# Kernel optimization log

Measured on AMD Instinct MI355X. Metric: run time of the kernel, lower is better.

## Reference

```python
import jax, jax.numpy as jnp
import numpy as np

N_NODES = 50000
N_EDGES = 400000
IN_SIZE = 64
HID = 128


def _graph_conv(x, src, dst, W, b, n_nodes):
    """dgl-style GraphConv: gather src features, mean-aggregate at dst, then Linear."""
    msgs = x[src]                                            # [E, F] irregular gather
    agg = jax.ops.segment_sum(msgs, dst, num_segments=n_nodes)  # [N, F]
    deg = jax.ops.segment_sum(jnp.ones_like(dst, dtype=x.dtype), dst,
                              num_segments=n_nodes)
    agg = agg / jnp.maximum(deg, 1.0)[:, None]               # mean over in-neighbors
    return agg @ W + b


def setup_inputs() -> dict:
    key = jax.random.key(0)
    k1, k2, k3, k4, k5 = jax.random.split(key, 5)
    inputs = jax.random.normal(k1, (N_NODES, IN_SIZE), dtype=jnp.float32)
    states = jax.random.normal(k2, (N_NODES, HID), dtype=jnp.float32)
    edge_index = jax.random.randint(k3, (2, N_EDGES), 0, N_NODES, dtype=jnp.int32)
    fin = IN_SIZE + HID
    s1 = 1.0 / np.sqrt(fin)
    W_ru = jax.random.uniform(k4, (fin, 2 * HID), minval=-s1, maxval=s1, dtype=jnp.float32)
    b_ru = jnp.zeros((2 * HID,), dtype=jnp.float32)
    W_c = jax.random.uniform(k5, (fin, HID), minval=-s1, maxval=s1, dtype=jnp.float32)
    b_c = jnp.zeros((HID,), dtype=jnp.float32)
    return {"inputs": inputs, "states": states, "edge_index": edge_index,
            "W_ru": W_ru, "b_ru": b_ru, "W_c": W_c, "b_c": b_c}


def reference(inputs, states, edge_index, W_ru, b_ru, W_c, b_c):
    n = inputs.shape[0]
    src, dst = edge_index[0], edge_index[1]
    # r,u gates
    ru_in = jnp.concatenate([inputs, states], axis=-1)        # [N, in+hid]
    r_u = jax.nn.sigmoid(_graph_conv(ru_in, src, dst, W_ru, b_ru, n))  # [N, 2*hid]
    r, u = jnp.split(r_u, 2, axis=-1)
    # candidate
    c_in = jnp.concatenate([inputs, r * states], axis=-1)
    c = jnp.tanh(_graph_conv(c_in, src, dst, W_c, b_c, n))    # [N, hid]
    new_state = u * states + (1.0 - u) * c
    return (new_state, new_state)
```

## Files before the change

kernel.cpp:

```cpp
#include <hip/hip_runtime.h>
#include <hip/hip_bf16.h>
#include <math.h>

#define N_NODES 50000
#define N_EDGES 400000
#define F_IN    64
#define HID     128
#define FIN     192
#define RU      256
#define BCAP    128

#define COUNTS_OFF 0u
#define BKT_OFF    200064u
#define WRU_OFF    13000064u
#define WC_OFF     13098368u
#define SBF_OFF    13147520u
#define AX_OFF     25947520u
#define AS_OFF     32347520u
#define ARS_OFF    45147520u
#define RS2_OFF    57947520u
#define WS_NEED    70747520u

typedef __attribute__((ext_vector_type(8))) short short8;
typedef __attribute__((ext_vector_type(4))) float f32x4;

__device__ __forceinline__ float sigf(float x) { return 1.f / (1.f + expf(-x)); }
__device__ __forceinline__ float bf2f(unsigned short h) {
    return __uint_as_float(((unsigned)h) << 16);
}
__device__ __forceinline__ float bflo(unsigned v) { return __uint_as_float(v << 16); }
__device__ __forceinline__ float bfhi(unsigned v) { return __uint_as_float(v & 0xffff0000u); }
__device__ __forceinline__ unsigned short f2bf(float f) {
    unsigned u = __float_as_uint(f);
    return (unsigned short)((u + 0x7fff + ((u >> 16) & 1)) >> 16);
}
__device__ __forceinline__ unsigned packbf(float lo, float hi) {
    return ((unsigned)f2bf(hi) << 16) | (unsigned)f2bf(lo);
}

__global__ void k_fillb(const int* __restrict__ src, const int* __restrict__ dst,
                        int* __restrict__ counts, unsigned short* __restrict__ bkt) {
    const int e = blockIdx.x * 256 + threadIdx.x;
    if (e < N_EDGES) {
        const int d = dst[e];
        const int pos = atomicAdd(&counts[d], 1);
        if (pos < BCAP) bkt[(size_t)d * BCAP + pos] = (unsigned short)src[e];
    }
}

__global__ __launch_bounds__(256) void k_pre(
        const float* __restrict__ Wru, const float* __restrict__ Wc,
        unsigned short* __restrict__ Wru_bf, unsigned short* __restrict__ Wc_bf,
        const float* __restrict__ states, const float* __restrict__ inputs,
        uint2* __restrict__ s_bf2, uint2* __restrict__ x_bf2) {
    const int blk = blockIdx.x;
    if (blk < 288) {
        const int t = blk * 256 + threadIdx.x;
        if (t < FIN * RU) {
            const int k = t >> 8, c = t & 255;
            Wru_bf[c * FIN + k] = f2bf(Wru[t]);
        } else {
            const int tt = t - FIN * RU;
            const int k = tt >> 7, c = tt & 127;
            Wc_bf[c * FIN + k] = f2bf(Wc[tt]);
        }
    } else {
        const int t = (blk - 288) * 256 + threadIdx.x;
        if (t < N_NODES * HID / 4) {
            const float4 v = ((const float4*)states)[t];
            s_bf2[t] = make_uint2(packbf(v.x, v.y), packbf(v.z, v.w));
        } else {
            const int j = t - N_NODES * HID / 4;
            const float4 v = ((const float4*)inputs)[j];
            x_bf2[j] = make_uint2(packbf(v.x, v.y), packbf(v.z, v.w));
        }
    }
}

__global__ __launch_bounds__(256) void k_agg1(
        const unsigned short* __restrict__ bkt, const int* __restrict__ counts,
        const unsigned* __restrict__ x_u, const uint2* __restrict__ s_u2,
        unsigned* __restrict__ Ax_u, uint2* __restrict__ As_u2) {
    const int n = blockIdx.x * 4 + (threadIdx.x >> 6);
    const int lane = threadIdx.x & 63;
    const int half = lane >> 5;
    const int l = lane & 31;
    const int deg   = counts[n];
    const int start = n * BCAP;
    const int end   = start + (deg < BCAP ? deg : BCAP);
    float ax0 = 0.f, ax1 = 0.f, s0 = 0.f, s1 = 0.f, s2 = 0.f, s3 = 0.f;
    int e = start;
    for (; e + 8 <= end; e += 8) {
        const int ia = bkt[e + half];
        const int ib = bkt[e + 2 + half];
        const int ic = bkt[e + 4 + half];
        const int id = bkt[e + 6 + half];
        const unsigned xa = x_u[(size_t)ia * 32 + l];
        const uint2    sa = s_u2[(size_t)ia * 32 + l];
        const unsigned xb = x_u[(size_t)ib * 32 + l];
        const uint2    sb = s_u2[(size_t)ib * 32 + l];
        const unsigned xc = x_u[(size_t)ic * 32 + l];
        const uint2    sc = s_u2[(size_t)ic * 32 + l];
        const unsigned xd = x_u[(size_t)id * 32 + l];
        const uint2    sd = s_u2[(size_t)id * 32 + l];
        ax0 += bflo(xa); ax1 += bfhi(xa);
        s0 += bflo(sa.x); s1 += bfhi(sa.x); s2 += bflo(sa.y); s3 += bfhi(sa.y);
        ax0 += bflo(xb); ax1 += bfhi(xb);
        s0 += bflo(sb.x); s1 += bfhi(sb.x); s2 += bflo(sb.y); s3 += bfhi(sb.y);
        ax0 += bflo(xc); ax1 += bfhi(xc);
        s0 += bflo(sc.x); s1 += bfhi(sc.x); s2 += bflo(sc.y); s3 += bfhi(sc.y);
        ax0 += bflo(xd); ax1 += bfhi(xd);
        s0 += bflo(sd.x); s1 += bfhi(sd.x); s2 += bflo(sd.y); s3 += bfhi(sd.y);
    }
    if (e + 4 <= end) {
        const int ia = bkt[e + half];
        const int ib = bkt[e + 2 + half];
        const unsigned xa = x_u[(size_t)ia * 32 + l];
        const uint2    sa = s_u2[(size_t)ia * 32 + l];
        const unsigned xb = x_u[(size_t)ib * 32 + l];
        const uint2    sb = s_u2[(size_t)ib * 32 + l];
        ax0 += bflo(xa); ax1 += bfhi(xa);
        s0 += bflo(sa.x); s1 += bfhi(sa.x); s2 += bflo(sa.y); s3 += bfhi(sa.y);
        ax0 += bflo(xb); ax1 += bfhi(xb);
        s0 += bflo(sb.x); s1 += bfhi(sb.x); s2 += bflo(sb.y); s3 += bfhi(sb.y);
        e += 4;
    }
    if (e + 2 <= end) {
        const int ia = bkt[e + half];
        const unsigned xa = x_u[(size_t)ia * 32 + l];
        const uint2    sa = s_u2[(size_t)ia * 32 + l];
        ax0 += bflo(xa); ax1 += bfhi(xa);
        s0 += bflo(sa.x); s1 += bfhi(sa.x); s2 += bflo(sa.y); s3 += bfhi(sa.y);
        e += 2;
    }
    if (e < end && half == 0) {
        const int ia = bkt[e];
        const unsigned xa = x_u[(size_t)ia * 32 + l];
        const uint2    sa = s_u2[(size_t)ia * 32 + l];
        ax0 += bflo(xa); ax1 += bfhi(xa);
        s0 += bflo(sa.x); s1 += bfhi(sa.x); s2 += bflo(sa.y); s3 += bfhi(sa.y);
    }
    ax0 += __shfl_xor(ax0, 32); ax1 += __shfl_xor(ax1, 32);
    s0  += __shfl_xor(s0, 32);  s1  += __shfl_xor(s1, 32);
    s2  += __shfl_xor(s2, 32);  s3  += __shfl_xor(s3, 32);
    if (half == 0) {
        const float inv = 1.f / fmaxf((float)deg, 1.f);
        Ax_u[(size_t)n * 32 + l]  = packbf(ax0 * inv, ax1 * inv);
        As_u2[(size_t)n * 32 + l] = make_uint2(packbf(s0 * inv, s1 * inv),
                                               packbf(s2 * inv, s3 * inv));
    }
}

__global__ __launch_bounds__(256) void k_agg2(
        const unsigned short* __restrict__ bkt, const int* __restrict__ counts,
        const uint2* __restrict__ rs_u2, uint2* __restrict__ Ars_u2) {
    const int n = blockIdx.x * 4 + (threadIdx.x >> 6);
    const int lane = threadIdx.x & 63;
    const int half = lane >> 5;
    const int l = lane & 31;
    const int deg   = counts[n];
    const int start = n * BCAP;
    const int end   = start + (deg < BCAP ? deg : BCAP);
    float a0 = 0.f, a1 = 0.f, a2 = 0.f, a3 = 0.f;
    int e = start;
    for (; e + 8 <= end; e += 8) {
        const int ia = bkt[e + half];
        const int ib = bkt[e + 2 + half];
        const int ic = bkt[e + 4 + half];
        const int id = bkt[e + 6 + half];
        const uint2 va = rs_u2[(size_t)ia * 32 + l];
        const uint2 vb = rs_u2[(size_t)ib * 32 + l];
        const uint2 vc = rs_u2[(size_t)ic * 32 + l];
        const uint2 vd = rs_u2[(size_t)id * 32 + l];
        a0 += bflo(va.x); a1 += bfhi(va.x); a2 += bflo(va.y); a3 += bfhi(va.y);
        a0 += bflo(vb.x); a1 += bfhi(vb.x); a2 += bflo(vb.y); a3 += bfhi(vb.y);
        a0 += bflo(vc.x); a1 += bfhi(vc.x); a2 += bflo(vc.y); a3 += bfhi(vc.y);
        a0 += bflo(vd.x); a1 += bfhi(vd.x); a2 += bflo(vd.y); a3 += bfhi(vd.y);
    }
    if (e + 4 <= end) {
        const int ia = bkt[e + half];
        const int ib = bkt[e + 2 + half];
        const uint2 va = rs_u2[(size_t)ia * 32 + l];
        const uint2 vb = rs_u2[(size_t)ib * 32 + l];
        a0 += bflo(va.x); a1 += bfhi(va.x); a2 += bflo(va.y); a3 += bfhi(va.y);
        a0 += bflo(vb.x); a1 += bfhi(vb.x); a2 += bflo(vb.y); a3 += bfhi(vb.y);
        e += 4;
    }
    if (e + 2 <= end) {
        const int ia = bkt[e + half];
        const uint2 va = rs_u2[(size_t)ia * 32 + l];
        a0 += bflo(va.x); a1 += bfhi(va.x); a2 += bflo(va.y); a3 += bfhi(va.y);
        e += 2;
    }
    if (e < end && half == 0) {
        const int ia = bkt[e];
        const uint2 va = rs_u2[(size_t)ia * 32 + l];
        a0 += bflo(va.x); a1 += bfhi(va.x); a2 += bflo(va.y); a3 += bfhi(va.y);
    }
    a0 += __shfl_xor(a0, 32); a1 += __shfl_xor(a1, 32);
    a2 += __shfl_xor(a2, 32); a3 += __shfl_xor(a3, 32);
    if (half == 0) {
        const float inv = 1.f / fmaxf((float)deg, 1.f);
        Ars_u2[(size_t)n * 32 + l] = make_uint2(packbf(a0 * inv, a1 * inv),
                                                packbf(a2 * inv, a3 * inv));
    }
}

__global__ __launch_bounds__(256, 4) void k_gemm_r(
        const unsigned short* __restrict__ Ax, const unsigned short* __restrict__ As,
        const unsigned short* __restrict__ Wbf, const float* __restrict__ b,
        const unsigned short* __restrict__ s_bf, unsigned short* __restrict__ rs2) {
    __shared__ unsigned short Wt[64][200];
    const int t  = threadIdx.x;
    const int n0 = blockIdx.x * 128;
    const int colbase = blockIdx.y * 64;

    #pragma unroll
    for (int it = 0; it < 6; ++it) {
        const int task = t + 256 * it;
        const int c = task / 24, g = task - c * 24;
        *(uint4*)(&Wt[c][g * 8]) =
            *(const uint4*)(Wbf + (size_t)(colbase + c) * FIN + g * 8);
    }

    const int lane = t & 63, wave = t >> 6;
    const int fr = lane & 15;
    const int fk = (lane >> 4) * 8;

    short8 afr[2][6];
    const short8 zero = {};
    #pragma unroll
    for (int s = 0; s < 2; ++s) {
        const int n = n0 + wave * 32 + s * 16 + fr;
        if (n < N_NODES) {
            const unsigned short* axp = Ax + (size_t)n * F_IN + fk;
            const unsigned short* asp = As + (size_t)n * HID + fk;
            afr[s][0] = *(const short8*)(axp);
            afr[s][1] = *(const short8*)(axp + 32);
            afr[s][2] = *(const short8*)(asp);
            afr[s][3] = *(const short8*)(asp + 32);
            afr[s][4] = *(const short8*)(asp + 64);
            afr[s][5] = *(const short8*)(asp + 96);
        } else {
            #pragma unroll
            for (int j = 0; j < 6; ++j) afr[s][j] = zero;
        }
    }
    __syncthreads();

    f32x4 acc[2][4] = {};
    #pragma unroll
    for (int k0 = 0; k0 < 6; ++k0) {
        #pragma unroll
        for (int ct = 0; ct < 4; ++ct) {
            const short8 bw = *(const short8*)(&Wt[ct * 16 + fr][fk + k0 * 32]);
            acc[0][ct] = __builtin_amdgcn_mfma_f32_16x16x32_bf16(afr[0][k0], bw, acc[0][ct], 0, 0, 0);
            acc[1][ct] = __builtin_amdgcn_mfma_f32_16x16x32_bf16(afr[1][k0], bw, acc[1][ct], 0, 0, 0);
        }
    }

    #pragma unroll
    for (int s = 0; s < 2; ++s) {
        const int rbase = n0 + wave * 32 + s * 16 + (lane >> 4) * 4;
        #pragma unroll
        for (int ct = 0; ct < 4; ++ct) {
            const int col = colbase + ct * 16 + fr;
            const float bias = b[col];
            #pragma unroll
            for (int i = 0; i < 4; ++i) {
                const int n = rbase + i;
                if (n < N_NODES) {
                    const size_t idx = (size_t)n * HID + col;
                    const float r = sigf(acc[s][ct][i] + bias);
                    rs2[idx] = f2bf(r * bf2f(s_bf[idx]));
                }
            }
        }
    }
}

__global__ __launch_bounds__(256) void k_gemm_uc(
        const unsigned short* __restrict__ Ax, const unsigned short* __restrict__ As,
        const unsigned short* __restrict__ Ars,
        const unsigned short* __restrict__ Wru_bf, const unsigned short* __restrict__ Wc_bf,
        const float* __restrict__ b_ru, const float* __restrict__ b_c,
        const unsigned short* __restrict__ st_bf,
        float* __restrict__ out1, float* __restrict__ out2) {
    __shared__ unsigned short Wt[64][200];
    const int t  = threadIdx.x;
    const int n0 = blockIdx.x * 64;
    const int colbase = blockIdx.y * 64;
    const int lane = t & 63, wave = t >> 6;
    const int fr = lane & 15;
    const int fk = (lane >> 4) * 8;
    const int n = n0 + wave * 16 + fr;
    const short8 zero = {};

    #pragma unroll
    for (int it = 0; it < 6; ++it) {
        const int task = t + 256 * it;
        const int c = task / 24, g = task - c * 24;
        *(uint4*)(&Wt[c][g * 8]) =
            *(const uint4*)(Wru_bf + (size_t)(128 + colbase + c) * FIN + g * 8);
    }

    short8 axf0 = zero, axf1 = zero, sf[4] = {zero, zero, zero, zero};
    if (n < N_NODES) {
        const unsigned short* axp = Ax + (size_t)n * F_IN + fk;
        const unsigned short* asp = As + (size_t)n * HID + fk;
        axf0 = *(const short8*)(axp);
        axf1 = *(const short8*)(axp + 32);
        sf[0] = *(const short8*)(asp);
        sf[1] = *(const short8*)(asp + 32);
        sf[2] = *(const short8*)(asp + 64);
        sf[3] = *(const short8*)(asp + 96);
    }
    __syncthreads();

    f32x4 uacc[4] = {};
    #pragma unroll
    for (int k0 = 0; k0 < 6; ++k0) {
        const short8 a = (k0 == 0) ? axf0 : (k0 == 1) ? axf1 : sf[k0 - 2];
        #pragma unroll
        for (int ct = 0; ct < 4; ++ct) {
            const short8 bw = *(const short8*)(&Wt[ct * 16 + fr][fk + k0 * 32]);
            uacc[ct] = __builtin_amdgcn_mfma_f32_16x16x32_bf16(a, bw, uacc[ct], 0, 0, 0);
        }
    }
    float uu[4][4];
    #pragma unroll
    for (int ct = 0; ct < 4; ++ct) {
        const float bias = b_ru[128 + colbase + ct * 16 + fr];
        #pragma unroll
        for (int i = 0; i < 4; ++i) uu[ct][i] = sigf(uacc[ct][i] + bias);
    }
    __syncthreads();

    #pragma unroll
    for (int it = 0; it < 6; ++it) {
        const int task = t + 256 * it;
        const int c = task / 24, g = task - c * 24;
        *(uint4*)(&Wt[c][g * 8]) =
            *(const uint4*)(Wc_bf + (size_t)(colbase + c) * FIN + g * 8);
    }
    if (n < N_NODES) {
        const unsigned short* arp = Ars + (size_t)n * HID + fk;
        sf[0] = *(const short8*)(arp);
        sf[1] = *(const short8*)(arp + 32);
        sf[2] = *(const short8*)(arp + 64);
        sf[3] = *(const short8*)(arp + 96);
    }
    __syncthreads();

    f32x4 cacc[4] = {};
    #pragma unroll
    for (int k0 = 0; k0 < 6; ++k0) {
        const short8 a = (k0 == 0) ? axf0 : (k0 == 1) ? axf1 : sf[k0 - 2];
        #pragma unroll
        for (int ct = 0; ct < 4; ++ct) {
            const short8 bw = *(const short8*)(&Wt[ct * 16 + fr][fk + k0 * 32]);
            cacc[ct] = __builtin_amdgcn_mfma_f32_16x16x32_bf16(a, bw, cacc[ct], 0, 0, 0);
        }
    }

    const int rbase = n0 + wave * 16 + (lane >> 4) * 4;
    #pragma unroll
    for (int ct = 0; ct < 4; ++ct) {
        const int col = colbase + ct * 16 + fr;
        const float bias = b_c[col];
        #pragma unroll
        for (int i = 0; i < 4; ++i) {
            const int nn = rbase + i;
            if (nn < N_NODES) {
                const size_t idx = (size_t)nn * HID + col;
                const float c  = tanhf(cacc[ct][i] + bias);
                const float u  = uu[ct][i];
                const float st = bf2f(st_bf[idx]);
                const float ns = u * st + (1.f - u) * c;
                out1[idx] = ns;
                out2[idx] = ns;
            }
        }
    }
}

extern "C" void kernel_launch(void* const* d_in, const int* in_sizes, int n_in,
                              void* d_out, int out_size, void* d_ws, size_t ws_size,
                              hipStream_t stream) {
    const float* inputs = (const float*)d_in[0];
    const float* states = (const float*)d_in[1];
    const int*   ei     = (const int*)d_in[2];
    const float* W_ru   = (const float*)d_in[3];
    const float* b_ru   = (const float*)d_in[4];
    const float* W_c    = (const float*)d_in[5];
    const float* b_c    = (const float*)d_in[6];

    float* out  = (float*)d_out;
    float* out1 = out;
    float* out2 = out + (size_t)N_NODES * HID;

    char* ws = (char*)d_ws;
    int*            counts = (int*)(ws + COUNTS_OFF);
    unsigned short* bkt    = (unsigned short*)(ws + BKT_OFF);
    unsigned short* Wru_bf = (unsigned short*)(ws + WRU_OFF);
    unsigned short* Wc_bf  = (unsigned short*)(ws + WC_OFF);
    unsigned short* s_bf   = (unsigned short*)(ws + SBF_OFF);
    unsigned short* Ax     = (unsigned short*)(ws + AX_OFF);
    unsigned short* As     = (unsigned short*)(ws + AS_OFF);
    unsigned short* Ars    = (unsigned short*)(ws + ARS_OFF);
    unsigned short* rs2    = (unsigned short*)(ws + RS2_OFF);
    unsigned short* x_bf   = (unsigned short*)d_out;

    (void)ws_size;

    const int* src = ei;
    const int* dst = ei + N_EDGES;

    const int egrid      = (N_EDGES + 255) / 256;
    const int agg_grid   = N_NODES / 4;
    const int gr_grid    = (N_NODES + 127) / 128;
    const int guc_grid   = (N_NODES + 63) / 64;
    const int pre_grid   = 288 + (N_NODES * HID / 4 + N_NODES * F_IN / 4) / 256;

    hipMemsetAsync(counts, 0, N_NODES * sizeof(int), stream);
    k_fillb <<<egrid, 256, 0, stream>>>(src, dst, counts, bkt);
    k_pre   <<<pre_grid, 256, 0, stream>>>(W_ru, W_c, Wru_bf, Wc_bf, states, inputs,
                                           (uint2*)s_bf, (uint2*)x_bf);
    k_agg1  <<<agg_grid, 256, 0, stream>>>(bkt, counts, (const unsigned*)x_bf,
                                           (const uint2*)s_bf,
                                           (unsigned*)Ax, (uint2*)As);
    k_gemm_r<<<dim3(gr_grid, 2), 256, 0, stream>>>(Ax, As, Wru_bf, b_ru, s_bf, rs2);
    k_agg2  <<<agg_grid, 256, 0, stream>>>(bkt, counts, (const uint2*)rs2,
                                           (uint2*)Ars);
    k_gemm_uc<<<dim3(guc_grid, 2), 256, 0, stream>>>(Ax, As, Ars, Wru_bf, Wc_bf,
                                                     b_ru, b_c, s_bf, out1, out2);
}
```

Before: 141.2 us.

## Fuse bucket fill with preconversion kernel; double rows per block in gate GEMM

Merges the edge-bucketing kernel and the weight/feature bf16 conversion kernel into one launch, partitioned by block index, to save a launch and let the two run concurrently. Also makes k_gemm_uc process 128 nodes per block (two 16-row subtiles per wave), reusing each LDS weight tile across twice as many rows and halving the number of weight staging loads. The wider tile raises register use, which the added occupancy hint of 3 blocks per CU is meant to keep in check, and it reuses the u accumulators to hold the sigmoid values.

```diff
diff --git a/kernel.cpp b/kernel.cpp
--- a/kernel.cpp
+++ b/kernel.cpp
@@ -21,6 +21,10 @@
 #define RS2_OFF    57947520u
 #define WS_NEED    70747520u
 
+#define FILLB_BLKS 1563
+#define PREW_BLKS  288
+#define PREP_BLKS  9375
+
 typedef __attribute__((ext_vector_type(8))) short short8;
 typedef __attribute__((ext_vector_type(4))) float f32x4;
 
@@ -38,24 +42,23 @@
     return ((unsigned)f2bf(hi) << 16) | (unsigned)f2bf(lo);
 }
 
-__global__ void k_fillb(const int* __restrict__ src, const int* __restrict__ dst,
-                        int* __restrict__ counts, unsigned short* __restrict__ bkt) {
-    const int e = blockIdx.x * 256 + threadIdx.x;
-    if (e < N_EDGES) {
-        const int d = dst[e];
-        const int pos = atomicAdd(&counts[d], 1);
-        if (pos < BCAP) bkt[(size_t)d * BCAP + pos] = (unsigned short)src[e];
-    }
-}
-
-__global__ __launch_bounds__(256) void k_pre(
+__global__ __launch_bounds__(256) void k_fp(
+        const int* __restrict__ src, const int* __restrict__ dst,
+        int* __restrict__ counts, unsigned short* __restrict__ bkt,
         const float* __restrict__ Wru, const float* __restrict__ Wc,
         unsigned short* __restrict__ Wru_bf, unsigned short* __restrict__ Wc_bf,
         const float* __restrict__ states, const float* __restrict__ inputs,
         uint2* __restrict__ s_bf2, uint2* __restrict__ x_bf2) {
     const int blk = blockIdx.x;
-    if (blk < 288) {
-        const int t = blk * 256 + threadIdx.x;
+    if (blk < FILLB_BLKS) {
+        const int e = blk * 256 + threadIdx.x;
+        if (e < N_EDGES) {
+            const int d = dst[e];
+            const int pos = atomicAdd(&counts[d], 1);
+            if (pos < BCAP) bkt[(size_t)d * BCAP + pos] = (unsigned short)src[e];
+        }
+    } else if (blk < FILLB_BLKS + PREW_BLKS) {
+        const int t = (blk - FILLB_BLKS) * 256 + threadIdx.x;
         if (t < FIN * RU) {
             const int k = t >> 8, c = t & 255;
             Wru_bf[c * FIN + k] = f2bf(Wru[t]);
@@ -65,7 +68,7 @@
             Wc_bf[c * FIN + k] = f2bf(Wc[tt]);
         }
     } else {
-        const int t = (blk - 288) * 256 + threadIdx.x;
+        const int t = (blk - FILLB_BLKS - PREW_BLKS) * 256 + threadIdx.x;
         if (t < N_NODES * HID / 4) {
             const float4 v = ((const float4*)states)[t];
             s_bf2[t] = make_uint2(packbf(v.x, v.y), packbf(v.z, v.w));
@@ -279,7 +282,7 @@
     }
 }
 
-__global__ __launch_bounds__(256) void k_gemm_uc(
+__global__ __launch_bounds__(256, 3) void k_gemm_uc(
         const unsigned short* __restrict__ Ax, const unsigned short* __restrict__ As,
         const unsigned short* __restrict__ Ars,
         const unsigned short* __restrict__ Wru_bf, const unsigned short* __restrict__ Wc_bf,
@@ -288,12 +291,11 @@
         float* __restrict__ out1, float* __restrict__ out2) {
     __shared__ unsigned short Wt[64][200];
     const int t  = threadIdx.x;
-    const int n0 = blockIdx.x * 64;
+    const int n0 = blockIdx.x * 128;
     const int colbase = blockIdx.y * 64;
     const int lane = t & 63, wave = t >> 6;
     const int fr = lane & 15;
     const int fk = (lane >> 4) * 8;
-    const int n = n0 + wave * 16 + fr;
     const short8 zero = {};
 
     #pragma unroll
@@ -304,36 +306,49 @@
             *(const uint4*)(Wru_bf + (size_t)(128 + colbase + c) * FIN + g * 8);
     }
 
-    short8 axf0 = zero, axf1 = zero, sf[4] = {zero, zero, zero, zero};
-    if (n < N_NODES) {
-        const unsigned short* axp = Ax + (size_t)n * F_IN + fk;
-        const unsigned short* asp = As + (size_t)n * HID + fk;
-        axf0 = *(const short8*)(axp);
-        axf1 = *(const short8*)(axp + 32);
-        sf[0] = *(const short8*)(asp);
-        sf[1] = *(const short8*)(asp + 32);
-        sf[2] = *(const short8*)(asp + 64);
-        sf[3] = *(const short8*)(asp + 96);
+    short8 axf[2][2], sf[2][4];
+    #pragma unroll
+    for (int s = 0; s < 2; ++s) {
+        const int n = n0 + wave * 32 + s * 16 + fr;
+        if (n < N_NODES) {
+            const unsigned short* axp = Ax + (size_t)n * F_IN + fk;
+            const unsigned short* asp = As + (size_t)n * HID + fk;
+            axf[s][0] = *(const short8*)(axp);
+            axf[s][1] = *(const short8*)(axp + 32);
+            sf[s][0] = *(const short8*)(asp);
+            sf[s][1] = *(const short8*)(asp + 32);
+            sf[s][2] = *(const short8*)(asp + 64);
+            sf[s][3] = *(const short8*)(asp + 96);
+        } else {
+            axf[s][0] = zero; axf[s][1] = zero;
+            #pragma unroll
+            for (int j = 0; j < 4; ++j) sf[s][j] = zero;
+        }
     }
     __syncthreads();
 
-    f32x4 uacc[4] = {};
+    f32x4 uacc[2][4] = {};
     #pragma unroll
     for (int k0 = 0; k0 < 6; ++k0) {
-        const short8 a = (k0 == 0) ? axf0 : (k0 == 1) ? axf1 : sf[k0 - 2];
+        #pragma unroll
+        for (int s = 0; s < 2; ++s) {
+            const short8 a = (k0 < 2) ? axf[s][k0] : sf[s][k0 - 2];
+            #pragma unroll
+            for (int ct = 0; ct < 4; ++ct) {
+                const short8 bw = *(const short8*)(&Wt[ct * 16 + fr][fk + k0 * 32]);
+                uacc[s][ct] = __builtin_amdgcn_mfma_f32_16x16x32_bf16(a, bw, uacc[s][ct], 0, 0, 0);
+            }
+        }
+    }
+    #pragma unroll
+    for (int s = 0; s < 2; ++s)
         #pragma unroll
         for (int ct = 0; ct < 4; ++ct) {
-            const short8 bw = *(const short8*)(&Wt[ct * 16 + fr][fk + k0 * 32]);
-            uacc[ct] = __builtin_amdgcn_mfma_f32_16x16x32_bf16(a, bw, uacc[ct], 0, 0, 0);
-        }
-    }
-    float uu[4][4];
-    #pragma unroll
-    for (int ct = 0; ct < 4; ++ct) {
-        const float bias = b_ru[128 + colbase + ct * 16 + fr];
-        #pragma unroll
-        for (int i = 0; i < 4; ++i) uu[ct][i] = sigf(uacc[ct][i] + bias);
-    }
+            const float bias = b_ru[128 + colbase + ct * 16 + fr];
+            #pragma unroll
+            for (int i = 0; i < 4; ++i)
+                uacc[s][ct][i] = sigf(uacc[s][ct][i] + bias);
+        }
     __syncthreads();
 
     #pragma unroll
@@ -343,42 +358,52 @@
         *(uint4*)(&Wt[c][g * 8]) =
             *(const uint4*)(Wc_bf + (size_t)(colbase + c) * FIN + g * 8);
     }
-    if (n < N_NODES) {
-        const unsigned short* arp = Ars + (size_t)n * HID + fk;
-        sf[0] = *(const short8*)(arp);
-        sf[1] = *(const short8*)(arp + 32);
-        sf[2] = *(const short8*)(arp + 64);
-        sf[3] = *(const short8*)(arp + 96);
+    #pragma unroll
+    for (int s = 0; s < 2; ++s) {
+        const int n = n0 + wave * 32 + s * 16 + fr;
+        if (n < N_NODES) {
+            const unsigned short* arp = Ars + (size_t)n * HID + fk;
+            sf[s][0] = *(const short8*)(arp);
+            sf[s][1] = *(const short8*)(arp + 32);
+            sf[s][2] = *(const short8*)(arp + 64);
+            sf[s][3] = *(const short8*)(arp + 96);
+        }
     }
     __syncthreads();
 
-    f32x4 cacc[4] = {};
+    f32x4 cacc[2][4] = {};
     #pragma unroll
     for (int k0 = 0; k0 < 6; ++k0) {
-        const short8 a = (k0 == 0) ? axf0 : (k0 == 1) ? axf1 : sf[k0 - 2];
+        #pragma unroll
+        for (int s = 0; s < 2; ++s) {
+            const short8 a = (k0 < 2) ? axf[s][k0] : sf[s][k0 - 2];
+            #pragma unroll
+            for (int ct = 0; ct < 4; ++ct) {
+                const short8 bw = *(const short8*)(&Wt[ct * 16 + fr][fk + k0 * 32]);
+                cacc[s][ct] = __builtin_amdgcn_mfma_f32_16x16x32_bf16(a, bw, cacc[s][ct], 0, 0, 0);
+            }
+        }
+    }
+
+    #pragma unroll
+    for (int s = 0; s < 2; ++s) {
+        const int rbase = n0 + wave * 32 + s * 16 + (lane >> 4) * 4;
         #pragma unroll
         for (int ct = 0; ct < 4; ++ct) {
-            const short8 bw = *(const short8*)(&Wt[ct * 16 + fr][fk + k0 * 32]);
-            cacc[ct] = __builtin_amdgcn_mfma_f32_16x16x32_bf16(a, bw, cacc[ct], 0, 0, 0);
-        }
-    }
-
-    const int rbase = n0 + wave * 16 + (lane >> 4) * 4;
-    #pragma unroll
-    for (int ct = 0; ct < 4; ++ct) {
-        const int col = colbase + ct * 16 + fr;
-        const float bias = b_c[col];
-        #pragma unroll
-        for (int i = 0; i < 4; ++i) {
-            const int nn = rbase + i;
-            if (nn < N_NODES) {
-                const size_t idx = (size_t)nn * HID + col;
-                const float c  = tanhf(cacc[ct][i] + bias);
-                const float u  = uu[ct][i];
-                const float st = bf2f(st_bf[idx]);
-                const float ns = u * st + (1.f - u) * c;
-                out1[idx] = ns;
-                out2[idx] = ns;
+            const int col = colbase + ct * 16 + fr;
+            const float bias = b_c[col];
+            #pragma unroll
+            for (int i = 0; i < 4; ++i) {
+                const int nn = rbase + i;
+                if (nn < N_NODES) {
+                    const size_t idx = (size_t)nn * HID + col;
+                    const float c  = tanhf(cacc[s][ct][i] + bias);
+                    const float u  = uacc[s][ct][i];
+                    const float st = bf2f(st_bf[idx]);
+                    const float ns = u * st + (1.f - u) * c;
+                    out1[idx] = ns;
+                    out2[idx] = ns;
+                }
             }
         }
     }
@@ -416,22 +441,20 @@
     const int* src = ei;
     const int* dst = ei + N_EDGES;
 
-    const int egrid      = (N_EDGES + 255) / 256;
-    const int agg_grid   = N_NODES / 4;
-    const int gr_grid    = (N_NODES + 127) / 128;
-    const int guc_grid   = (N_NODES + 63) / 64;
-    const int pre_grid   = 288 + (N_NODES * HID / 4 + N_NODES * F_IN / 4) / 256;
+    const int agg_grid = N_NODES / 4;
+    const int gr_grid  = (N_NODES + 127) / 128;
+    const int fp_grid  = FILLB_BLKS + PREW_BLKS + PREP_BLKS;
 
     hipMemsetAsync(counts, 0, N_NODES * sizeof(int), stream);
-    k_fillb <<<egrid, 256, 0, stream>>>(src, dst, counts, bkt);
-    k_pre   <<<pre_grid, 256, 0, stream>>>(W_ru, W_c, Wru_bf, Wc_bf, states, inputs,
-                                           (uint2*)s_bf, (uint2*)x_bf);
+    k_fp    <<<fp_grid, 256, 0, stream>>>(src, dst, counts, bkt, W_ru, W_c,
+                                          Wru_bf, Wc_bf, states, inputs,
+                                          (uint2*)s_bf, (uint2*)x_bf);
     k_agg1  <<<agg_grid, 256, 0, stream>>>(bkt, counts, (const unsigned*)x_bf,
                                            (const uint2*)s_bf,
                                            (unsigned*)Ax, (uint2*)As);
     k_gemm_r<<<dim3(gr_grid, 2), 256, 0, stream>>>(Ax, As, Wru_bf, b_ru, s_bf, rs2);
     k_agg2  <<<agg_grid, 256, 0, stream>>>(bkt, counts, (const uint2*)rs2,
                                            (uint2*)Ars);
-    k_gemm_uc<<<dim3(guc_grid, 2), 256, 0, stream>>>(Ax, As, Ars, Wru_bf, Wc_bf,
-                                                     b_ru, b_c, s_bf, out1, out2);
-}
+    k_gemm_uc<<<dim3(gr_grid, 2), 256, 0, stream>>>(Ax, As, Ars, Wru_bf, Wc_bf,
+                                                    b_ru, b_c, s_bf, out1, out2);
+}
```

Result: slower. 148.3 us (+5.0%).
